# Kernel optimization log

Hardware: AMD Instinct MI355X
Metric: run time of the kernel (lower is better)

## Reference

```python
import jax, jax.numpy as jnp
import numpy as np

NEG = -1e9
N_HEADS = 8

def layer_norm(x, scale, bias, eps=1e-7):
    m = x.mean(-1, keepdims=True)
    v = jnp.var(x, axis=-1, keepdims=True)
    return (x - m) * jax.lax.rsqrt(v + eps) * scale + bias

def attention(x, wqkv, wo, mask):
    B, S, H = x.shape
    dh = H // N_HEADS
    q, k, v = jnp.split(x @ wqkv, 3, axis=-1)
    hsplit = lambda t: t.reshape(B, S, N_HEADS, dh).transpose(0, 2, 1, 3)
    q, k, v = hsplit(q), hsplit(k), hsplit(v)
    scores = jnp.einsum('bhqd,bhkd->bhqk', q, k) / jnp.sqrt(jnp.float32(dh))
    probs = jax.nn.softmax(scores + mask, axis=-1)
    out = jnp.einsum('bhqk,bhkd->bhqd', probs, v).transpose(0, 2, 1, 3).reshape(B, S, H)
    return out @ wo

def encoder(x, mask, wqkv, wo, ln1, w1, w2, ln2):
    for l in range(wqkv.shape[0]):  # small fixed layer count
        x = layer_norm(x + attention(x, wqkv[l], wo[l], mask), ln1[l, 0], ln1[l, 1])
        h = jax.nn.gelu(x @ w1[l]) @ w2[l]
        x = layer_norm(x + h, ln2[l, 0], ln2[l, 1])
    return x

def setup_inputs() -> dict:
    key = jax.random.key(0)
    B, C, T, H, F, L, V = 2, 16, 64, 512, 2048, 2, 32000
    ks = iter(jax.random.split(key, 64))
    nrm = lambda shape, s=0.02: jax.random.normal(next(ks), shape, jnp.float32) * s
    lnp = lambda: jnp.stack([jnp.ones(H, jnp.float32), jnp.zeros(H, jnp.float32)])
    lnL = lambda: jnp.broadcast_to(jnp.stack([jnp.ones(H, jnp.float32), jnp.zeros(H, jnp.float32)]), (L, 2, H)) + 0.0
    num_tokens = jax.random.randint(next(ks), (B, C), 2, T + 1)
    num_chunks = jax.random.randint(next(ks), (B,), C // 2, C + 1)
    raw_ids = jax.random.randint(next(ks), (B, C, T), 1, V)
    token_ids = jnp.where(jnp.arange(T)[None, None, :] < num_tokens[:, :, None], raw_ids, 0)
    def tf(pfx):
        return {pfx + '_wqkv': nrm((L, H, 3 * H)), pfx + '_wo': nrm((L, H, H)), pfx + '_ln1': lnL(),
                pfx + '_w1': nrm((L, H, F)), pfx + '_w2': nrm((L, F, H)), pfx + '_ln2': lnL()}
    d = {'token_ids': token_ids, 'num_chunks': num_chunks, 'num_tokens': num_tokens,
         'tok_emb': nrm((V, H)), 'tok_emb_ln': lnp(), 'chunk_pos': nrm((C, H)), 'chunk_emb_ln': lnp(),
         'sos': nrm((H,)), 'dec_emb': nrm((V, H)), 'dec_emb_ln': lnp(),
         'cls_dense': nrm((H, H)), 'cls_ln': lnp(), 'cls_proj': nrm((H, V)), 'cls_b': jnp.zeros((V,), jnp.float32)}
    d.update(tf('tok')); d.update(tf('chk')); d.update(tf('dec'))
    return d

def reference(token_ids, num_chunks, num_tokens, tok_emb, tok_emb_ln, tok_wqkv, tok_wo, tok_ln1, tok_w1, tok_w2, tok_ln2, chunk_pos, chunk_emb_ln, chk_wqkv, chk_wo, chk_ln1, chk_w1, chk_w2, chk_ln2, sos, dec_emb, dec_emb_ln, dec_wqkv, dec_wo, dec_ln1, dec_w1, dec_w2, dec_ln2, cls_dense, cls_ln, cls_proj, cls_b):
    B, C, T = token_ids.shape
    H = sos.shape[0]
    S2 = C + T
    # --- token encoder over stacked chunks [B*C, T] ---
    ids = token_ids.reshape(B * C, T)
    tok_valid = jnp.arange(T)[None, :] < num_tokens.reshape(B * C, 1)
    tok_amask = jnp.where(tok_valid, 0.0, NEG)[:, None, None, :]
    x = layer_norm(tok_emb[ids], tok_emb_ln[0], tok_emb_ln[1])
    token_units = encoder(x, tok_amask, tok_wqkv, tok_wo, tok_ln1, tok_w1, tok_w2, tok_ln2)
    # --- chunk encoder (patched causal): CLS unit per chunk + chunk position embs ---
    chunk_embs = token_units.reshape(B, C, T, H)[:, :, 0, :] + chunk_pos[None]
    chunk_embs = layer_norm(chunk_embs, chunk_emb_ln[0], chunk_emb_ln[1])
    chunk_valid = jnp.arange(C)[None, :] < num_chunks[:, None]  # [B,C]
    chk_amask = jnp.where(jnp.tril(jnp.ones((C, C), bool))[None] & chunk_valid[:, None, :], 0.0, NEG)[:, None]
    chunk_units = encoder(chunk_embs, chk_amask, chk_wqkv, chk_wo, chk_ln1, chk_w1, chk_w2, chk_ln2)
    chunk_units_sos = jnp.concatenate([jnp.broadcast_to(sos, (B, 1, H)), chunk_units[:, :-1]], axis=1)
    # --- ragged decoder-input assembly (vectorized scatter replacing the double python loop) ---
    dec_tok_embs = layer_norm(dec_emb[token_ids], dec_emb_ln[0], dec_emb_ln[1])  # [B,C,T,H]
    p = jnp.arange(S2); c = jnp.arange(C); n = num_tokens
    cond_prefix = (p[None, None, :] <= c[None, :, None]) & chunk_valid[:, :, None]            # [B,C,S2]
    cond_tok = (p[None, None, :] > c[None, :, None]) & (p[None, None, :] <= c[None, :, None] + n[:, :, None]) & chunk_valid[:, :, None]
    prefix = chunk_units_sos[:, jnp.minimum(p, C - 1)]                                        # [B,S2,H]
    tidx = jnp.clip(p[None, :] - c[:, None] - 1, 0, T - 1)                                    # [C,S2]
    tok_part = jnp.take_along_axis(dec_tok_embs, jnp.broadcast_to(tidx[None, :, :, None], (B, C, S2, 1)), axis=2)
    dec_in = jnp.where(cond_prefix[..., None], prefix[:, None], 0.0) + jnp.where(cond_tok[..., None], tok_part, 0.0)
    # --- causal decoder over [B*C, C+T, H] ---
    dec_amask = jnp.where(jnp.tril(jnp.ones((S2, S2), bool)), 0.0, NEG)[None, None]
    units = encoder(dec_in.reshape(B * C, S2, H), dec_amask, dec_wqkv, dec_wo, dec_ln1, dec_w1, dec_w2, dec_ln2)
    units = units.reshape(B, C, S2, H)
    # --- ragged reassembly (vectorized gather replacing the double python loop) ---
    t = jnp.arange(T - 1)
    ridx = c[:, None] + 1 + t[None, :]  # [C,T-1], always < C+T
    gathered = jnp.take_along_axis(units, jnp.broadcast_to(ridx[None, :, :, None], (B, C, T - 1, 1)), axis=2)
    rmask = (t[None, None, :] < n[:, :, None] - 1) & chunk_valid[:, :, None]
    units_re = jnp.where(rmask[..., None], gathered, 0.0)
    # --- MLM head (cls): dense + gelu + LN + vocab projection ---
    y = layer_norm(jax.nn.gelu(units_re @ cls_dense), cls_ln[0], cls_ln[1])
    logits = y @ cls_proj + cls_b  # [B,C,T-1,V]
    return logits
```

## Files before the change

### kernel.cpp

```cpp
#include <hip/hip_runtime.h>
#include <hip/hip_bf16.h>


typedef __hip_bfloat16 bf16;
typedef __attribute__((ext_vector_type(8))) short short8;
typedef __attribute__((ext_vector_type(4))) float f32x4;

__device__ inline float b2f(bf16 x) { return __bfloat162float(x); }
__device__ inline bf16 f2b(float x) { return __float2bfloat16(x); }
__device__ inline short f2bs(float x) { bf16 h = __float2bfloat16(x); return *reinterpret_cast<short*>(&h); }
__device__ inline float gelu_f(float x) {
    return 0.5f * x * (1.f + tanhf(0.7978845608028654f * (x + 0.044715f * x * x * x)));
}
__device__ __forceinline__ void gload16(const void* g, void* l) {
    __builtin_amdgcn_global_load_lds(
        (const __attribute__((address_space(1))) unsigned int*)g,
        (__attribute__((address_space(3))) unsigned int*)l, 16, 0, 0);
}

#define NMAT 26
struct TAll {
    const float* src[NMAT];
    bf16* dst[NMAT];
    int K[NMAT], N[NMAT];
    int ofs[NMAT + 1];
};

__global__ __launch_bounds__(256) void k_transpose(TAll ta) {
    __shared__ float tile[32][33];
    int bid = blockIdx.x;
    int m = 0;
    while (m + 1 < NMAT && bid >= ta.ofs[m + 1]) ++m;
    int local = bid - ta.ofs[m];
    int K = ta.K[m], N = ta.N[m];
    int tilesX = N >> 5;
    int tx = local % tilesX, ty = local / tilesX;
    int k0 = ty << 5, n0 = tx << 5;
    const float* src = ta.src[m];
    bf16* dst = ta.dst[m];
    int t = threadIdx.x;
    int c = t & 31, r = t >> 5;
#pragma unroll
    for (int p = 0; p < 4; ++p)
        tile[r + p * 8][c] = src[(long)(k0 + r + p * 8) * N + n0 + c];
    __syncthreads();
#pragma unroll
    for (int p = 0; p < 4; ++p)
        dst[(long)(n0 + r + p * 8) * K + k0 + c] = __float2bfloat16(tile[c][r + p * 8]);
}

template<int BM, int BN, int ACT, int BIAS, int OUTBF, int VT = 0, int SWZ = 0>
__global__ __launch_bounds__(256) void k_gemm_mfma(const bf16* __restrict__ A,
        const bf16* __restrict__ Bt, const float* __restrict__ bias,
        void* __restrict__ Cc, int M, int N, int K, bf16* __restrict__ vt, int S) {
    constexpr int WM = BM / 2, WN = BN / 2, FM = WM / 16, FN = WN / 16;
    constexpr int L = BM / 32 + BN / 32;
    constexpr int ASZ = BM * 64, BSZ = BN * 64;
    __shared__ __align__(16) short As[2 * ASZ];
    __shared__ __align__(16) short Bs[2 * BSZ];
    int m0, n0;
    if constexpr (SWZ) {
        int pI = blockIdx.y * 16 + blockIdx.x;
        int q = pI >> 7, r = pI & 127;
        int mt = r >> 3, nt = q * 8 + (r & 7);
        if (nt * BN >= N) return;
        m0 = mt * BM; n0 = nt * BN;
    } else {
        m0 = blockIdx.y * BM; n0 = blockIdx.x * BN;
    }
    int tid = threadIdx.x;
    int w = tid >> 6, l = tid & 63;
    int wm = w >> 1, wn = w & 1;
    int l16 = l & 15, kg = l >> 4;
    int srow = l >> 3, scol = (l & 7) * 16;
    f32x4 acc[FM][FN];
#pragma unroll
    for (int i = 0; i < FM; ++i)
#pragma unroll
        for (int j = 0; j < FN; ++j) acc[i][j] = 0.f;

    auto stage = [&](int kt, int half) {
        long kof = (long)kt * 64;
#pragma unroll
        for (int p = 0; p < BM / 32; ++p) {
            int r = p * 32 + w * 8 + srow;
            gload16((const char*)A + (((long)(m0 + r) * K + kof) << 1) + (scol ^ ((r & 7) << 4)),
                    (char*)As + half * (ASZ * 2) + (p * 32 + w * 8) * 128);
        }
#pragma unroll
        for (int p = 0; p < BN / 32; ++p) {
            int r = p * 32 + w * 8 + srow;
            gload16((const char*)Bt + (((long)(n0 + r) * K + kof) << 1) + (scol ^ ((r & 7) << 4)),
                    (char*)Bs + half * (BSZ * 2) + (p * 32 + w * 8) * 128);
        }
    };

    int NT = K >> 6;
    stage(0, 0);
    for (int t = 0; t < NT; ++t) {
        int cur = t & 1;
        if (t + 1 < NT) {
            stage(t + 1, cur ^ 1);
            if constexpr (L == 3)      asm volatile("s_waitcnt vmcnt(3)" ::: "memory");
            else if constexpr (L == 4) asm volatile("s_waitcnt vmcnt(4)" ::: "memory");
            else if constexpr (L == 6) asm volatile("s_waitcnt vmcnt(6)" ::: "memory");
            else                       asm volatile("s_waitcnt vmcnt(8)" ::: "memory");
        } else {
            asm volatile("s_waitcnt vmcnt(0)" ::: "memory");
        }
        __builtin_amdgcn_s_barrier();
        const char* Ab = (const char*)As + cur * (ASZ * 2);
        const char* Bb = (const char*)Bs + cur * (BSZ * 2);
#pragma unroll
        for (int ks = 0; ks < 2; ++ks) {
            short8 a[FM], b[FN];
#pragma unroll
            for (int i = 0; i < FM; ++i) {
                int ar = wm * WM + i * 16 + l16;
                a[i] = *reinterpret_cast<const short8*>(Ab + ar * 128 + ((ks * 64 + kg * 16) ^ ((ar & 7) << 4)));
            }
#pragma unroll
            for (int j = 0; j < FN; ++j) {
                int br = wn * WN + j * 16 + l16;
                b[j] = *reinterpret_cast<const short8*>(Bb + br * 128 + ((ks * 64 + kg * 16) ^ ((br & 7) << 4)));
            }
#pragma unroll
            for (int i = 0; i < FM; ++i)
#pragma unroll
                for (int j = 0; j < FN; ++j)
                    acc[i][j] = __builtin_amdgcn_mfma_f32_16x16x32_bf16(a[i], b[j], acc[i][j], 0, 0, 0);
        }
        asm volatile("s_waitcnt lgkmcnt(0)" ::: "memory");
        __builtin_amdgcn_sched_barrier(0);
        __builtin_amdgcn_s_barrier();
    }
#pragma unroll
    for (int i = 0; i < FM; ++i) {
#pragma unroll
        for (int jj = 0; jj < 4; ++jj) {
            int row = m0 + wm * WM + i * 16 + kg * 4 + jj;
            if (row < M) {
#pragma unroll
                for (int j = 0; j < FN; ++j) {
                    int col = n0 + wn * WN + j * 16 + l16;
                    float v = acc[i][j][jj];
                    if (BIAS) v += bias[col];
                    if (ACT) v = gelu_f(v);
                    if (VT && col >= 1024) {
                        int hh = (col - 1024) >> 6, dd = (col - 1024) & 63;
                        int sq = row / S, key = row - sq * S;
                        int SPl = ((S + 31) >> 5) << 5;
                        vt[(((long)sq * 8 + hh) * 64 + dd) * SPl + key] = f2b(v);
                    } else if (OUTBF) {
                        ((bf16*)Cc)[(long)row * N + col] = f2b(v);
                    } else {
                        ((float*)Cc)[(long)row * N + col] = v;
                    }
                }
            }
        }
    }
}

template<int S>
__global__ __launch_bounds__(64) void k_attn_mfma(const bf16* __restrict__ qkv,
        const bf16* __restrict__ vt, bf16* __restrict__ att,
        const int* __restrict__ limits, int causal) {
    constexpr int KT = S / 16;
    constexpr int SP = ((S + 31) / 32) * 32;
    constexpr int KS = SP / 32;
    constexpr int SPAD = SP - KT * 16;
    __shared__ __align__(16) short Pw[16 * 104];
    int bid = blockIdx.x;
    int qt = bid % KT;
    int bh = bid / KT;
    int h = bh & 7, seq = bh >> 3;
    int l = threadIdx.x;
    int l16 = l & 15, kg = l >> 4;
    int lim = limits ? limits[seq] : S;
    const short* qk = (const short*)qkv + (long)seq * S * 1536 + h * 64;
    const short* vb_base = (const short*)vt + ((long)(seq * 8 + h) * 64) * SP;

    f32x4 sc[KT];
#pragma unroll
    for (int kt = 0; kt < KT; ++kt) sc[kt] = 0.f;
#pragma unroll
    for (int ks = 0; ks < 2; ++ks) {
        short8 qa = *reinterpret_cast<const short8*>(qk + (long)(qt * 16 + l16) * 1536 + ks * 32 + kg * 8);
#pragma unroll
        for (int kt = 0; kt < KT; ++kt) {
            short8 kb = *reinterpret_cast<const short8*>(qk + (long)(kt * 16 + l16) * 1536 + 512 + ks * 32 + kg * 8);
            sc[kt] = __builtin_amdgcn_mfma_f32_16x16x32_bf16(qa, kb, sc[kt], 0, 0, 0);
        }
    }
#pragma unroll
    for (int jj = 0; jj < 4; ++jj) {
        int q = qt * 16 + kg * 4 + jj;
        float vs[KT], m = -1e30f;
#pragma unroll
        for (int kt = 0; kt < KT; ++kt) {
            int key = kt * 16 + l16;
            float s = sc[kt][jj] * 0.125f;
            bool ok = (!causal || key <= q) && (key < lim);
            vs[kt] = ok ? s : -1e30f;
            m = fmaxf(m, vs[kt]);
        }
#pragma unroll
        for (int o = 1; o < 16; o <<= 1) m = fmaxf(m, __shfl_xor(m, o));
        float sum = 0.f;
#pragma unroll
        for (int kt = 0; kt < KT; ++kt) { vs[kt] = __expf(vs[kt] - m); sum += vs[kt]; }
#pragma unroll
        for (int o = 1; o < 16; o <<= 1) sum += __shfl_xor(sum, o);
        float rinv = 1.f / sum;
#pragma unroll
        for (int kt = 0; kt < KT; ++kt)
            Pw[(kg * 4 + jj) * 104 + kt * 16 + l16] = f2bs(vs[kt] * rinv);
    }
    if (SPAD > 0) {
#pragma unroll
        for (int jj = 0; jj < 4; ++jj)
            Pw[(kg * 4 + jj) * 104 + KT * 16 + l16] = 0;
    }
    f32x4 ao[4];
#pragma unroll
    for (int ct = 0; ct < 4; ++ct) ao[ct] = 0.f;
#pragma unroll
    for (int kst = 0; kst < KS; ++kst) {
        short8 pa = *reinterpret_cast<const short8*>((const char*)Pw + l16 * 208 + kst * 64 + kg * 16);
#pragma unroll
        for (int ct = 0; ct < 4; ++ct) {
            short8 vbf = *reinterpret_cast<const short8*>(vb_base + (long)(ct * 16 + l16) * SP + kst * 32 + kg * 8);
            ao[ct] = __builtin_amdgcn_mfma_f32_16x16x32_bf16(pa, vbf, ao[ct], 0, 0, 0);
        }
    }
#pragma unroll
    for (int ct = 0; ct < 4; ++ct)
#pragma unroll
        for (int jj = 0; jj < 4; ++jj) {
            int q = qt * 16 + kg * 4 + jj;
            att[((long)seq * S + q) * 512 + h * 64 + ct * 16 + l16] = f2b(ao[ct][jj]);
        }
}

__device__ inline void ln_finish(float v0, float v1, const float* __restrict__ lnw,
                                 bf16* __restrict__ outrow) {
    float s = v0 + v1, q = v0 * v0 + v1 * v1;
#pragma unroll
    for (int o = 32; o > 0; o >>= 1) { s += __shfl_xor(s, o); q += __shfl_xor(q, o); }
    __shared__ float rs[4], rq[4];
    int w = threadIdx.x >> 6;
    if ((threadIdx.x & 63) == 0) { rs[w] = s; rq[w] = q; }
    __syncthreads();
    s = rs[0] + rs[1] + rs[2] + rs[3];
    q = rq[0] + rq[1] + rq[2] + rq[3];
    float m = s * (1.f / 512.f);
    float var = q * (1.f / 512.f) - m * m;
    float inv = rsqrtf(var + 1e-7f);
    int i0 = threadIdx.x * 2, i1 = i0 + 1;
    outrow[i0] = f2b((v0 - m) * inv * lnw[i0] + lnw[512 + i0]);
    outrow[i1] = f2b((v1 - m) * inv * lnw[i1] + lnw[512 + i1]);
}

__global__ __launch_bounds__(256) void k_embed_ln2(const int* __restrict__ ids,
        const float* __restrict__ tok_emb, const float* __restrict__ tok_lnw,
        const float* __restrict__ dec_emb, const float* __restrict__ dec_lnw,
        bf16* __restrict__ x, bf16* __restrict__ dec_tok) {
    int row = blockIdx.x;
    const float* emb; const float* lnw; bf16* out;
    if (row < 2048) { emb = tok_emb; lnw = tok_lnw; out = x + (long)row * 512; }
    else { row -= 2048; emb = dec_emb; lnw = dec_lnw; out = dec_tok + (long)row * 512; }
    const float* e = emb + (long)ids[row] * 512;
    int i0 = threadIdx.x * 2;
    ln_finish(e[i0], e[i0 + 1], lnw, out);
}

__global__ __launch_bounds__(256) void k_add_ln(const bf16* __restrict__ a, const bf16* __restrict__ b,
        const float* __restrict__ lnw, bf16* __restrict__ out) {
    int row = blockIdx.x;
    long off = (long)row * 512;
    int i0 = threadIdx.x * 2;
    float v0 = b2f(a[off + i0]), v1 = b2f(a[off + i0 + 1]);
    if (b) { v0 += b2f(b[off + i0]); v1 += b2f(b[off + i0 + 1]); }
    ln_finish(v0, v1, lnw, out + off);
}

__global__ __launch_bounds__(256) void k_chunk_ln(const bf16* __restrict__ tu, const float* __restrict__ cpos,
        const float* __restrict__ lnw, bf16* __restrict__ out) {
    int bc = blockIdx.x;
    int c = bc & 15;
    long toff = (long)bc * 64 * 512;
    int i0 = threadIdx.x * 2;
    float v0 = b2f(tu[toff + i0])     + cpos[c * 512 + i0];
    float v1 = b2f(tu[toff + i0 + 1]) + cpos[c * 512 + i0 + 1];
    ln_finish(v0, v1, lnw, out + (long)bc * 512);
}

__global__ __launch_bounds__(256) void k_dec_in(const bf16* __restrict__ chunk_units,
        const float* __restrict__ sos, const bf16* __restrict__ dec_tok,
        const int* __restrict__ num_chunks, const int* __restrict__ num_tokens,
        bf16* __restrict__ out) {
    int row = blockIdx.x;
    int p = row % 80;
    int bc = row / 80;
    int c = bc & 15, b = bc >> 4;
    int t = threadIdx.x;
    bf16* o = out + (long)row * 512;
    if (c < num_chunks[b]) {
        if (p <= c) {
            if (p == 0) {
                o[2 * t]     = f2b(sos[2 * t]);
                o[2 * t + 1] = f2b(sos[2 * t + 1]);
                return;
            }
            ((uint*)o)[t] = ((const uint*)(chunk_units + ((long)(b * 16 + p - 1)) * 512))[t];
            return;
        }
        int n = num_tokens[bc];
        if (p <= c + n) {
            ((uint*)o)[t] = ((const uint*)(dec_tok + ((long)bc * 64 + (p - c - 1)) * 512))[t];
            return;
        }
    }
    ((uint*)o)[t] = 0u;
}

__global__ __launch_bounds__(256) void k_head_gather(const bf16* __restrict__ units,
        const int* __restrict__ num_chunks, const int* __restrict__ num_tokens,
        bf16* __restrict__ out) {
    int row = blockIdx.x;
    int t = row % 63;
    int bc = row / 63;
    int c = bc & 15, b = bc >> 4;
    bool valid = (c < num_chunks[b]) && (t < num_tokens[bc] - 1);
    uint* o = (uint*)(out + (long)row * 512);
    if (valid) {
        o[threadIdx.x] = ((const uint*)(units + ((long)bc * 80 + (c + 1 + t)) * 512))[threadIdx.x];
    } else {
        o[threadIdx.x] = 0u;
    }
}

template<int S>
static void run_encoder(hipStream_t st, bf16* x, int nseq, const int* limits, int causal,
                        bf16* const* wts, const float* ln1, const float* ln2,
                        bf16* qkv, bf16* vt, bf16* att, bf16* proj, bf16* x2, bf16* h1) {
    constexpr int KT = S / 16;
    int R = nseq * S;
    int gy64 = (R + 63) / 64, gy32 = (R + 31) / 32;
    for (int l = 0; l < 2; ++l) {
        k_gemm_mfma<64, 64, 0, 0, 1, 1><<<dim3(24, gy64), 256, 0, st>>>(x, wts[l * 4 + 0], nullptr, qkv, R, 1536, 512, vt, S);
        k_attn_mfma<S><<<dim3(nseq * 8 * KT), 64, 0, st>>>(qkv, vt, att, limits, causal);
        k_gemm_mfma<32, 64, 0, 0, 1><<<dim3(8, gy32), 256, 0, st>>>(att, wts[l * 4 + 1], nullptr, proj, R, 512, 512, nullptr, 0);
        k_add_ln<<<dim3(R), 256, 0, st>>>(x, proj, ln1 + (long)l * 1024, x2);
        k_gemm_mfma<64, 64, 1, 0, 1><<<dim3(32, gy64), 256, 0, st>>>(x2, wts[l * 4 + 2], nullptr, h1, R, 2048, 512, nullptr, 0);
        k_gemm_mfma<32, 64, 0, 0, 1><<<dim3(8, gy32), 256, 0, st>>>(h1, wts[l * 4 + 3], nullptr, proj, R, 512, 2048, nullptr, 0);
        k_add_ln<<<dim3(R), 256, 0, st>>>(x2, proj, ln2 + (long)l * 1024, x);
    }
}

extern "C" void kernel_launch(void* const* d_in, const int* in_sizes, int n_in,
                              void* d_out, int out_size, void* d_ws, size_t ws_size,
                              hipStream_t stream) {
    (void)in_sizes; (void)n_in; (void)out_size; (void)ws_size;
    const int*   token_ids    = (const int*)d_in[0];
    const int*   num_chunks   = (const int*)d_in[1];
    const int*   num_tokens   = (const int*)d_in[2];
    const float* tok_emb      = (const float*)d_in[3];
    const float* tok_emb_ln   = (const float*)d_in[4];
    const float* chunk_pos    = (const float*)d_in[5];
    const float* chunk_emb_ln = (const float*)d_in[6];
    const float* sos          = (const float*)d_in[7];
    const float* dec_emb      = (const float*)d_in[8];
    const float* dec_emb_ln   = (const float*)d_in[9];
    const float* cls_dense    = (const float*)d_in[10];
    const float* cls_ln       = (const float*)d_in[11];
    const float* cls_proj     = (const float*)d_in[12];
    const float* cls_b        = (const float*)d_in[13];
    const float* w_in[3][4] = {
        {(const float*)d_in[14], (const float*)d_in[15], (const float*)d_in[17], (const float*)d_in[18]},
        {(const float*)d_in[20], (const float*)d_in[21], (const float*)d_in[23], (const float*)d_in[24]},
        {(const float*)d_in[26], (const float*)d_in[27], (const float*)d_in[29], (const float*)d_in[30]},
    };
    const float* ln_in[3][2] = {
        {(const float*)d_in[16], (const float*)d_in[19]},
        {(const float*)d_in[22], (const float*)d_in[25]},
        {(const float*)d_in[28], (const float*)d_in[31]},
    };

    char* p = (char*)d_ws;
    auto carve_b = [&](size_t elems) {
        bf16* r = (bf16*)p;
        p += ((elems * 2 + 255) / 256) * 256;
        return r;
    };
    bf16* x       = carve_b((size_t)2560 * 512);
    bf16* qkv     = carve_b((size_t)2560 * 1536);
    bf16* vt      = carve_b((size_t)32 * 8 * 64 * 96);
    bf16* att     = carve_b((size_t)2560 * 512);
    bf16* proj    = carve_b((size_t)2560 * 512);
    bf16* x2      = carve_b((size_t)2560 * 512);
    bf16* h1      = carve_b((size_t)2560 * 2048);
    bf16* chunk_x = carve_b((size_t)64 * 512);
    bf16* dec_tok = carve_b((size_t)2048 * 512);
    bf16* unitsre = carve_b((size_t)2048 * 512);
    bf16* hbuf    = carve_b((size_t)2048 * 512);
    bf16* ybuf    = carve_b((size_t)2048 * 512);

    TAll ta;
    int nm = 0, tiles = 0;
    auto push = [&](const float* src, int K, int N) -> bf16* {
        bf16* dst = carve_b((size_t)K * N);
        ta.src[nm] = src; ta.dst[nm] = dst; ta.K[nm] = K; ta.N[nm] = N;
        ta.ofs[nm] = tiles;
        tiles += (K / 32) * (N / 32);
        ++nm;
        return dst;
    };
    static const int KN[4][2] = {{512, 1536}, {512, 512}, {512, 2048}, {2048, 512}};
    bf16* wt[3][8];
    for (int tf = 0; tf < 3; ++tf)
        for (int l = 0; l < 2; ++l)
            for (int m = 0; m < 4; ++m) {
                int K = KN[m][0], N = KN[m][1];
                wt[tf][l * 4 + m] = push(w_in[tf][m] + (long)l * K * N, K, N);
            }
    bf16* wt_dense = push(cls_dense, 512, 512);
    bf16* wt_proj  = push(cls_proj, 512, 32000);
    ta.ofs[nm] = tiles;

    k_transpose<<<dim3(tiles), 256, 0, stream>>>(ta);

    k_embed_ln2<<<4096, 256, 0, stream>>>(token_ids, tok_emb, tok_emb_ln, dec_emb, dec_emb_ln, x, dec_tok);

    run_encoder<64>(stream, x, 32, num_tokens, 0, wt[0], ln_in[0][0], ln_in[0][1],
                    qkv, vt, att, proj, x2, h1);
    k_chunk_ln<<<32, 256, 0, stream>>>(x, chunk_pos, chunk_emb_ln, chunk_x);
    run_encoder<16>(stream, chunk_x, 2, num_chunks, 1, wt[1], ln_in[1][0], ln_in[1][1],
                    qkv, vt, att, proj, x2, h1);
    k_dec_in<<<2560, 256, 0, stream>>>(chunk_x, sos, dec_tok, num_chunks, num_tokens, x);
    run_encoder<80>(stream, x, 32, nullptr, 1, wt[2], ln_in[2][0], ln_in[2][1],
                    qkv, vt, att, proj, x2, h1);
    k_head_gather<<<2016, 256, 0, stream>>>(x, num_chunks, num_tokens, unitsre);
    k_gemm_mfma<32, 64, 1, 0, 1><<<dim3(8, 63), 256, 0, stream>>>(unitsre, wt_dense, nullptr, hbuf, 2016, 512, 512, nullptr, 0);
    k_add_ln<<<2016, 256, 0, stream>>>(hbuf, nullptr, cls_ln, ybuf);
    k_gemm_mfma<128, 64, 0, 1, 0, 0, 1><<<dim3(16, 504), 256, 0, stream>>>(ybuf, wt_proj, cls_b, d_out, 2016, 32000, 512, nullptr, 0);
}
```

Measured before the change: 603.5 us.

## Replace LDS-staged vocab projection GEMM with direct-from-global MFMA kernel

Adds a dedicated GEMM kernel for the large vocabulary projection. Each wave loads its A and B fragments straight from global memory into registers, with no LDS staging, and works on 128x128 block tiles instead of 128x64. The grouped tile swizzle moves from the generic template into the new kernel. The aim is to remove LDS traffic and barrier overhead and raise per-block reuse, at the cost of uncoalesced 16-byte global loads that depend on L2/cache hits for the reuse that LDS used to provide.

```diff
diff --git a/kernel.cpp b/kernel.cpp
--- a/kernel.cpp
+++ b/kernel.cpp
@@ -49,7 +49,60 @@
         dst[(long)(n0 + r + p * 8) * K + k0 + c] = __float2bfloat16(tile[c][r + p * 8]);
 }
 
-template<int BM, int BN, int ACT, int BIAS, int OUTBF, int VT = 0, int SWZ = 0>
+__global__ __launch_bounds__(256) void k_gemm_direct(const bf16* __restrict__ A,
+        const bf16* __restrict__ Bt, const float* __restrict__ bias,
+        float* __restrict__ Cc, int M, int N, int K) {
+    int pI = blockIdx.y * 16 + blockIdx.x;
+    int q = pI >> 7, r = pI & 127;
+    int mt = r >> 3, nt = q * 8 + (r & 7);
+    if (nt * 128 >= N) return;
+    int tid = threadIdx.x;
+    int w = tid >> 6, l = tid & 63;
+    int wm = w >> 1, wn = w & 1;
+    int l16 = l & 15, kg = l >> 4;
+    int m0 = mt * 128 + wm * 64, n0 = nt * 128 + wn * 64;
+    const char* Ab = (const char*)A + ((long)(m0 + l16) * K + kg * 8) * 2;
+    const char* Bb = (const char*)Bt + ((long)(n0 + l16) * K + kg * 8) * 2;
+    long rstep = (long)16 * K * 2;
+    f32x4 acc[4][4];
+#pragma unroll
+    for (int i = 0; i < 4; ++i)
+#pragma unroll
+        for (int j = 0; j < 4; ++j) acc[i][j] = 0.f;
+
+    int NS = K >> 5;
+#pragma unroll 4
+    for (int ks = 0; ks < NS; ++ks) {
+        short8 a[4], b[4];
+#pragma unroll
+        for (int i = 0; i < 4; ++i)
+            a[i] = *reinterpret_cast<const short8*>(Ab + i * rstep + ks * 64);
+#pragma unroll
+        for (int j = 0; j < 4; ++j)
+            b[j] = *reinterpret_cast<const short8*>(Bb + j * rstep + ks * 64);
+#pragma unroll
+        for (int i = 0; i < 4; ++i)
+#pragma unroll
+            for (int j = 0; j < 4; ++j)
+                acc[i][j] = __builtin_amdgcn_mfma_f32_16x16x32_bf16(a[i], b[j], acc[i][j], 0, 0, 0);
+    }
+#pragma unroll
+    for (int i = 0; i < 4; ++i) {
+#pragma unroll
+        for (int jj = 0; jj < 4; ++jj) {
+            int row = m0 + i * 16 + kg * 4 + jj;
+            if (row < M) {
+#pragma unroll
+                for (int j = 0; j < 4; ++j) {
+                    int col = n0 + j * 16 + l16;
+                    Cc[(long)row * N + col] = acc[i][j][jj] + bias[col];
+                }
+            }
+        }
+    }
+}
+
+template<int BM, int BN, int ACT, int BIAS, int OUTBF, int VT = 0>
 __global__ __launch_bounds__(256) void k_gemm_mfma(const bf16* __restrict__ A,
         const bf16* __restrict__ Bt, const float* __restrict__ bias,
         void* __restrict__ Cc, int M, int N, int K, bf16* __restrict__ vt, int S) {
@@ -58,16 +111,7 @@
     constexpr int ASZ = BM * 64, BSZ = BN * 64;
     __shared__ __align__(16) short As[2 * ASZ];
     __shared__ __align__(16) short Bs[2 * BSZ];
-    int m0, n0;
-    if constexpr (SWZ) {
-        int pI = blockIdx.y * 16 + blockIdx.x;
-        int q = pI >> 7, r = pI & 127;
-        int mt = r >> 3, nt = q * 8 + (r & 7);
-        if (nt * BN >= N) return;
-        m0 = mt * BM; n0 = nt * BN;
-    } else {
-        m0 = blockIdx.y * BM; n0 = blockIdx.x * BN;
-    }
+    int m0 = blockIdx.y * BM, n0 = blockIdx.x * BN;
     int tid = threadIdx.x;
     int w = tid >> 6, l = tid & 63;
     int wm = w >> 1, wn = w & 1;
@@ -444,5 +488,5 @@
     k_head_gather<<<2016, 256, 0, stream>>>(x, num_chunks, num_tokens, unitsre);
     k_gemm_mfma<32, 64, 1, 0, 1><<<dim3(8, 63), 256, 0, stream>>>(unitsre, wt_dense, nullptr, hbuf, 2016, 512, 512, nullptr, 0);
     k_add_ln<<<2016, 256, 0, stream>>>(hbuf, nullptr, cls_ln, ybuf);
-    k_gemm_mfma<128, 64, 0, 1, 0, 0, 1><<<dim3(16, 504), 256, 0, stream>>>(ybuf, wt_proj, cls_b, d_out, 2016, 32000, 512, nullptr, 0);
-}
+    k_gemm_direct<<<dim3(16, 256), 256, 0, stream>>>(ybuf, wt_proj, cls_b, (float*)d_out, 2016, 32000, 512);
+}
```

After: 709.5 us. 17.6% more time.

## Stage GEMM epilogues through LDS for vectorized logits and V-transpose stores

Applied to the files above, without the earlier changes.

The vocabulary-projection GEMM moves to a 128x128 tile and gains an epilogue that stages fp32 accumulators in padded shared memory. Each row is then written back with coalesced float4 stores and a vectorized bias load, instead of scattered scalar stores from the MFMA layout. The QKV GEMM's V-transpose output is also staged through shared memory, so pairs of keys are packed and written as 32-bit words along the transposed dimension. The goal is to cut store inefficiency on the large logits write. The cost is a larger shared-memory footprint, which may lower occupancy, plus an extra barrier. The V path assumes a 64-row tile and even sequence lengths.

```diff
diff --git a/kernel.cpp b/kernel.cpp
--- a/kernel.cpp
+++ b/kernel.cpp
@@ -49,15 +49,21 @@
         dst[(long)(n0 + r + p * 8) * K + k0 + c] = __float2bfloat16(tile[c][r + p * 8]);
 }
 
-template<int BM, int BN, int ACT, int BIAS, int OUTBF, int VT = 0, int SWZ = 0>
+template<int BM, int BN, int ACT, int BIAS, int OUTBF, int VT = 0, int SWZ = 0, int EPIF32 = 0>
 __global__ __launch_bounds__(256) void k_gemm_mfma(const bf16* __restrict__ A,
         const bf16* __restrict__ Bt, const float* __restrict__ bias,
         void* __restrict__ Cc, int M, int N, int K, bf16* __restrict__ vt, int S) {
     constexpr int WM = BM / 2, WN = BN / 2, FM = WM / 16, FN = WN / 16;
     constexpr int L = BM / 32 + BN / 32;
     constexpr int ASZ = BM * 64, BSZ = BN * 64;
-    __shared__ __align__(16) short As[2 * ASZ];
-    __shared__ __align__(16) short Bs[2 * BSZ];
+    constexpr int SB = (ASZ + BSZ) * 2 * 2;
+    constexpr int EBf = EPIF32 ? BM * (BN + 4) * 4 : 0;
+    constexpr int EBv = VT ? 64 * 69 * 4 : 0;
+    constexpr int SMEM = SB > EBf ? (SB > EBv ? SB : EBv) : (EBf > EBv ? EBf : EBv);
+    __shared__ __align__(16) char smem[SMEM];
+    short* As = (short*)smem;
+    short* Bs = (short*)smem + 2 * ASZ;
+
     int m0, n0;
     if constexpr (SWZ) {
         int pI = blockIdx.y * 16 + blockIdx.x;
@@ -134,6 +140,60 @@
         __builtin_amdgcn_sched_barrier(0);
         __builtin_amdgcn_s_barrier();
     }
+
+    if constexpr (EPIF32) {
+        static_assert(BN == 128, "EPIF32 assumes BN=128");
+        float* T = (float*)smem;
+        constexpr int LDT = BN + 4;
+#pragma unroll
+        for (int i = 0; i < FM; ++i)
+#pragma unroll
+            for (int j = 0; j < FN; ++j)
+#pragma unroll
+                for (int jj = 0; jj < 4; ++jj)
+                    T[(wm * WM + i * 16 + kg * 4 + jj) * LDT + wn * WN + j * 16 + l16] = acc[i][j][jj];
+        __syncthreads();
+#pragma unroll
+        for (int it = 0; it < BM / 8; ++it) {
+            int rr = w * (BM / 4) + it * 2 + (l >> 5);
+            int row = m0 + rr;
+            int col = (l & 31) * 4;
+            float4 v = *reinterpret_cast<const float4*>(&T[rr * LDT + col]);
+            if (BIAS) {
+                float4 bb = *reinterpret_cast<const float4*>(&bias[n0 + col]);
+                v.x += bb.x; v.y += bb.y; v.z += bb.z; v.w += bb.w;
+            }
+            if (row < M)
+                *reinterpret_cast<float4*>(&((float*)Cc)[(long)row * N + n0 + col]) = v;
+        }
+        return;
+    }
+    if constexpr (VT) {
+        if (n0 >= 1024) {
+            float* T = (float*)smem;
+#pragma unroll
+            for (int i = 0; i < FM; ++i)
+#pragma unroll
+                for (int j = 0; j < FN; ++j)
+#pragma unroll
+                    for (int jj = 0; jj < 4; ++jj)
+                        T[(wm * WM + i * 16 + kg * 4 + jj) * 69 + wn * WN + j * 16 + l16] = acc[i][j][jj];
+            __syncthreads();
+            int h = (n0 - 1024) >> 6;
+            int SPl = ((S + 31) >> 5) << 5;
+#pragma unroll
+            for (int it = 0; it < 8; ++it) {
+                int d = w * 16 + it * 2 + (l >> 5);
+                int lr = (l & 31) * 2;
+                int g = m0 + lr;
+                int sq = g / S, key = g - sq * S;
+                uint pk = (uint)(unsigned short)f2bs(T[lr * 69 + d]) |
+                          ((uint)(unsigned short)f2bs(T[(lr + 1) * 69 + d]) << 16);
+                *reinterpret_cast<uint*>(vt + (((long)(sq * 8 + h) * 64 + d) * SPl + key)) = pk;
+            }
+            return;
+        }
+    }
 #pragma unroll
     for (int i = 0; i < FM; ++i) {
 #pragma unroll
@@ -146,16 +206,8 @@
                     float v = acc[i][j][jj];
                     if (BIAS) v += bias[col];
                     if (ACT) v = gelu_f(v);
-                    if (VT && col >= 1024) {
-                        int hh = (col - 1024) >> 6, dd = (col - 1024) & 63;
-                        int sq = row / S, key = row - sq * S;
-                        int SPl = ((S + 31) >> 5) << 5;
-                        vt[(((long)sq * 8 + hh) * 64 + dd) * SPl + key] = f2b(v);
-                    } else if (OUTBF) {
-                        ((bf16*)Cc)[(long)row * N + col] = f2b(v);
-                    } else {
-                        ((float*)Cc)[(long)row * N + col] = v;
-                    }
+                    if (OUTBF) ((bf16*)Cc)[(long)row * N + col] = f2b(v);
+                    else       ((float*)Cc)[(long)row * N + col] = v;
                 }
             }
         }
@@ -444,5 +496,5 @@
     k_head_gather<<<2016, 256, 0, stream>>>(x, num_chunks, num_tokens, unitsre);
     k_gemm_mfma<32, 64, 1, 0, 1><<<dim3(8, 63), 256, 0, stream>>>(unitsre, wt_dense, nullptr, hbuf, 2016, 512, 512, nullptr, 0);
     k_add_ln<<<2016, 256, 0, stream>>>(hbuf, nullptr, cls_ln, ybuf);
-    k_gemm_mfma<128, 64, 0, 1, 0, 0, 1><<<dim3(16, 504), 256, 0, stream>>>(ybuf, wt_proj, cls_b, d_out, 2016, 32000, 512, nullptr, 0);
-}
+    k_gemm_mfma<128, 128, 0, 1, 0, 0, 1, 1><<<dim3(16, 256), 256, 0, stream>>>(ybuf, wt_proj, cls_b, d_out, 2016, 32000, 512, nullptr, 0);
+}
```

Measured after the change: 499.8 us. 17.2% less time.
